# Kernel optimization log

Measured on AMD Instinct MI355X. Metric: run time of the kernel, lower is better.

## Reference

```python
import jax, jax.numpy as jnp
import numpy as np

N = 50000      # nodes
E = 800000     # edges (avg degree 16)
F = 80         # hidden_channels (forced by Linear(80, 1))
L = 4          # num_layers
NG = 1024      # graphs in batch
NFEAT = 9      # OGB atom feature columns
VOCAB = 119    # max atom feature vocab
EPS_BN = 1e-5
EPS_STD = 1e-5


def setup_inputs() -> dict:
    key = jax.random.key(0)
    ks = jax.random.split(key, 20)
    s = 0.05
    x = jax.random.randint(ks[0], (N, NFEAT), 0, 2)
    edge_index = jax.random.randint(ks[1], (2, E), 0, N)
    batch = jnp.sort(jax.random.randint(ks[2], (N,), 0, NG))
    # avg_deg['log'] from the degree histogram == mean over nodes of log(deg+1)
    deg = jax.ops.segment_sum(jnp.ones((E,), jnp.float32), edge_index[1], num_segments=N)
    avg_deg_log = jnp.array([jnp.mean(jnp.log(deg + 1.0))], jnp.float32)
    atom_emb = jax.random.normal(ks[3], (NFEAT, VOCAB, F), jnp.float32) * s
    pre_W = jax.random.normal(ks[4], (L, 2 * F, F), jnp.float32) * s
    pre_b = jax.random.normal(ks[5], (L, F), jnp.float32) * s
    post_W = jax.random.normal(ks[6], (L, 13 * F, F), jnp.float32) * s
    post_b = jax.random.normal(ks[7], (L, F), jnp.float32) * s
    lin_W = jax.random.normal(ks[8], (L, F, F), jnp.float32) * s
    lin_b = jax.random.normal(ks[9], (L, F), jnp.float32) * s
    bn_gamma = 1.0 + jax.random.normal(ks[10], (L, F), jnp.float32) * 0.1
    bn_beta = jax.random.normal(ks[11], (L, F), jnp.float32) * 0.1
    bn_mean = jax.random.normal(ks[12], (L, F), jnp.float32) * 0.1
    bn_var = 0.5 + jax.random.uniform(ks[13], (L, F), jnp.float32)
    mlp_W = jax.random.normal(ks[14], (F, 1), jnp.float32) * s
    mlp_b = jax.random.normal(ks[15], (1,), jnp.float32) * s
    return {
        'x': x, 'edge_index': edge_index, 'batch': batch,
        'avg_deg_log': avg_deg_log, 'atom_emb': atom_emb,
        'pre_W': pre_W, 'pre_b': pre_b, 'post_W': post_W, 'post_b': post_b,
        'lin_W': lin_W, 'lin_b': lin_b,
        'bn_gamma': bn_gamma, 'bn_beta': bn_beta, 'bn_mean': bn_mean, 'bn_var': bn_var,
        'mlp_W': mlp_W, 'mlp_b': mlp_b,
    }


def _forward(x, edge_index, batch, avg_deg_log, atom_emb, pre_W, pre_b,
             post_W, post_b, lin_W, lin_b, bn_gamma, bn_beta, bn_mean, bn_var,
             mlp_W, mlp_b):
    # AtomEncoder: sum of per-column embeddings
    h = jnp.sum(atom_emb[jnp.arange(NFEAT)[None, :], x], axis=1)  # [N, F]
    src, dst = edge_index[0], edge_index[1]
    deg = jax.ops.segment_sum(jnp.ones((E,), h.dtype), dst, num_segments=N)
    has_edge = (deg > 0)[:, None]
    degc = jnp.maximum(deg, 1.0)[:, None]          # clamp(min=1)
    logd = jnp.log(degc + 1.0)                     # [N, 1]
    avg = avg_deg_log[0]
    for i in range(L):
        x_h = h
        # message: pre_nn(cat([x_i, x_j]))
        m = jnp.concatenate([h[dst], h[src]], axis=-1) @ pre_W[i] + pre_b[i]  # [E, F]
        s1 = jax.ops.segment_sum(m, dst, num_segments=N)
        s2 = jax.ops.segment_sum(m * m, dst, num_segments=N)
        mean = s1 / degc
        var = s2 / degc - mean * mean
        std = jnp.sqrt(jax.nn.relu(var) + EPS_STD)
        mn = jnp.where(has_edge, jax.ops.segment_min(m, dst, num_segments=N), 0.0)
        mx = jnp.where(has_edge, jax.ops.segment_max(m, dst, num_segments=N), 0.0)
        agg = jnp.concatenate([mean, mn, mx, std], axis=-1)  # [N, 4F]
        sc = logd / avg
        out = jnp.concatenate([agg, agg * sc, agg / sc], axis=-1)  # [N, 12F]
        out = jnp.concatenate([h, out], axis=-1) @ post_W[i] + post_b[i]  # [N, F]
        out = out @ lin_W[i] + lin_b[i]
        out = (out - bn_mean[i]) * (bn_gamma[i] / jnp.sqrt(bn_var[i] + EPS_BN)) + bn_beta[i]
        h = x_h + jax.nn.relu(out)  # dropout is identity in eval
    counts = jnp.maximum(jax.ops.segment_sum(jnp.ones((N,), h.dtype), batch, num_segments=NG), 1.0)
    g = jax.ops.segment_sum(h, batch, num_segments=NG) / counts[:, None]  # global_mean_pool
    return g @ mlp_W + mlp_b  # [NG, 1]


def reference(x, edge_index, batch, avg_deg_log, atom_emb, pre_W, pre_b,
              post_W, post_b, lin_W, lin_b, bn_gamma, bn_beta, bn_mean, bn_var,
              mlp_W, mlp_b):
    return _forward(x, edge_index, batch, avg_deg_log, atom_emb, pre_W, pre_b,
                    post_W, post_b, lin_W, lin_b, bn_gamma, bn_beta, bn_mean, bn_var,
                    mlp_W, mlp_b)
```

## Files before the change

### kernel.cpp

```cpp
#include <hip/hip_runtime.h>
#include <hip/hip_bf16.h>

#define NN 50000
#define NE 800000
#define FD 80
#define NGR 1024
#define NF 9

#define BSH 6
#define NBUCK ((NN + 63) >> 6)
#define CSH 10
#define NCH ((NE + 1023) >> 10)
#define BCAP 2048

using bf16 = __hip_bfloat16;
typedef __attribute__((ext_vector_type(8))) short bf16x8;
typedef __attribute__((ext_vector_type(4))) float f32x4;

static __device__ __forceinline__ float b2f(bf16 v){ return __bfloat162float(v); }
static __device__ __forceinline__ bf16 f2b(float v){ return __float2bfloat16(v); }
static __device__ __forceinline__ float rdw(const void* p, int i, int fl){
  return fl ? ((const float*)p)[i] : b2f(((const bf16*)p)[i]);
}
static __device__ __forceinline__ unsigned pk(float a, float b){
  bf16 x = f2b(a), y = f2b(b);
  return (unsigned)*(unsigned short*)&x | ((unsigned)*(unsigned short*)&y << 16);
}
static __device__ __forceinline__ bf16x8 ldsld8(const short* p){
  union { bf16x8 v; uint2 u[2]; } r;
  r.u[0] = *(const uint2*)(p);
  r.u[1] = *(const uint2*)(p + 4);
  return r.v;
}
static __device__ __forceinline__ void ldsst16(short* p, uint4 v){
  *(uint2*)(p)     = make_uint2(v.x, v.y);
  *(uint2*)(p + 4) = make_uint2(v.z, v.w);
}

__global__ void k_zero(int* __restrict__ p, int n){
  int t = blockIdx.x*256 + threadIdx.x;
  if (t < n) p[t] = 0;
}

__global__ void k_probe(const void* __restrict__ emb, int* __restrict__ flag){
  int t = blockIdx.x*256 + threadIdx.x;
  float v = b2f(((const bf16*)emb)[t]);
  if (!(fabsf(v) < 1e4f)) atomicOr(flag, 1);
}

__global__ __launch_bounds__(256) void k_prep_all(
    const void* __restrict__ preW, const void* __restrict__ preb,
    const void* __restrict__ postW, const void* __restrict__ postb,
    const void* __restrict__ linW, const void* __restrict__ linb,
    const void* __restrict__ bng, const void* __restrict__ bnb,
    const void* __restrict__ bnm, const void* __restrict__ bnv,
    const int* __restrict__ flag,
    bf16* __restrict__ pwb, bf16* __restrict__ Btl, bf16* __restrict__ Bt1,
    float* __restrict__ bias1, float* __restrict__ bias2)
{
  int fl = flag[0];
  int b = blockIdx.x;
  if (b < 1300){
    int t = b*256 + threadIdx.x;
    pwb[t] = f2b(rdw(postW, t, fl));
  } else if (b < 1420){
    int t = (b - 1300)*256 + threadIdx.x;
    int j = t % 96, c = (t/96) % 80, i = t/(96*80);
    float v = 0.f;
    if (j < 80){
      float gs = rdw(bng, i*80 + c, fl) * rsqrtf(rdw(bnv, i*80 + c, fl) + 1e-5f);
      v = rdw(linW, i*6400 + j*80 + c, fl) * gs;
    }
    Btl[t] = f2b(v);
  } else if (b < 1660){
    int t = (b - 1420)*256 + threadIdx.x;
    int k = t % 96, c = (t/96) % 160, i = t/(96*160);
    float v = 0.f;
    if (k < 80)
      v = (c < 80) ? rdw(preW, (i*160 + k)*80 + c, fl)
                   : rdw(preW, (i*160 + 80 + k)*80 + (c - 80), fl);
    Bt1[t] = f2b(v);
    if (k == 0) bias1[i*160 + c] = (c < 80) ? rdw(preb, i*80 + c, fl) : 0.f;
  } else {
    int t = (b - 1660)*256 + threadIdx.x;
    if (t >= 4*80) return;
    int i = t / 80, f = t - i*80;
    float s = 0.f;
    for (int j = 0; j < 80; j++)
      s += rdw(postb, i*80 + j, fl) * rdw(linW, (i*80 + j)*80 + f, fl);
    s += rdw(linb, t, fl);
    float gs = rdw(bng, t, fl) * rsqrtf(rdw(bnv, t, fl) + 1e-5f);
    bias2[t] = (s - rdw(bnm, t, fl)) * gs + rdw(bnb, t, fl);
  }
}

__global__ void k_prep_Bt2(const float* __restrict__ Wf, bf16* __restrict__ Bt2){
  int t = blockIdx.x*256 + threadIdx.x;
  if (t >= 4*240*416) return;
  int k = t % 416;
  int c = (t/416) % 240;
  int i = t/(416*240);
  float v = 0.f;
  if (k < 400){
    int blk = c/80, f = c - blk*80;
    if (blk == 0) v = Wf[(i*1040 + k)*80 + f];
    else if (k >= 80){
      int row = (blk == 1 ? 400 : 720) + (k - 80);
      v = Wf[(i*1040 + row)*80 + f];
    }
  }
  Bt2[t] = f2b(v);
}

__global__ void k_atom(const int* __restrict__ x, const void* __restrict__ emb,
                       const int* __restrict__ flag, float* __restrict__ h){
  int fl = flag[0];
  int gid = blockIdx.x*256 + threadIdx.x;
  if (gid >= NN*FD) return;
  int n = gid / FD, f = gid - n*FD;
  float s = 0.f;
  #pragma unroll
  for (int c = 0; c < NF; c++){
    int row = x[n*NF + c];
    s += rdw(emb, (c*119 + row)*FD + f, fl);
  }
  h[gid] = s;
}


__global__ __launch_bounds__(256) void k_hist(const int* __restrict__ ei,
                                              int* __restrict__ chunkcnt){
  __shared__ int hist[NBUCK];
  int c = blockIdx.x, t = threadIdx.x;
  for (int i = t; i < NBUCK; i += 256) hist[i] = 0;
  __syncthreads();
  #pragma unroll
  for (int j = 0; j < 4; j++){
    int e = (c << CSH) + j*256 + t;
    if (e < NE) atomicAdd(&hist[ei[NE + e] >> BSH], 1);
  }
  __syncthreads();
  for (int i = t; i < NBUCK; i += 256) chunkcnt[c*NBUCK + i] = hist[i];
}

__global__ __launch_bounds__(256) void k_cscan(int* __restrict__ chunkcnt,
                                               int* __restrict__ btotal){
  __shared__ int buf[256];
  int b = blockIdx.x, t = threadIdx.x;
  int v[4]; int s = 0;
  #pragma unroll
  for (int j = 0; j < 4; j++){
    int c = t*4 + j;
    v[j] = (c < NCH) ? chunkcnt[c*NBUCK + b] : 0;
    s += v[j];
  }
  buf[t] = s;
  __syncthreads();
  for (int off = 1; off < 256; off <<= 1){
    int xv = (t >= off) ? buf[t - off] : 0;
    __syncthreads();
    buf[t] += xv;
    __syncthreads();
  }
  int excl = buf[t] - s;
  #pragma unroll
  for (int j = 0; j < 4; j++){
    int c = t*4 + j;
    if (c < NCH){ chunkcnt[c*NBUCK + b] = excl; excl += v[j]; }
  }
  if (t == 255) btotal[b] = buf[255];
}

__global__ __launch_bounds__(256) void k_bscan(const int* __restrict__ btotal,
                                               int* __restrict__ bbase){
  __shared__ int buf[256];
  int t = threadIdx.x;
  int v[4]; int s = 0;
  #pragma unroll
  for (int j = 0; j < 4; j++){
    int c = t*4 + j;
    v[j] = (c < NBUCK) ? btotal[c] : 0;
    s += v[j];
  }
  buf[t] = s;
  __syncthreads();
  for (int off = 1; off < 256; off <<= 1){
    int xv = (t >= off) ? buf[t - off] : 0;
    __syncthreads();
    buf[t] += xv;
    __syncthreads();
  }
  int excl = buf[t] - s;
  #pragma unroll
  for (int j = 0; j < 4; j++){
    int c = t*4 + j;
    if (c < NBUCK){ bbase[c] = excl; excl += v[j]; }
  }
  if (t == 255) bbase[NBUCK] = buf[255];
}

__global__ __launch_bounds__(256) void k_place(const int* __restrict__ ei,
                        const int* __restrict__ chunkcnt, const int* __restrict__ bbase,
                        int* __restrict__ staging){
  __shared__ int basep[NBUCK];
  __shared__ int cur[NBUCK];
  int c = blockIdx.x, t = threadIdx.x;
  for (int i = t; i < NBUCK; i += 256){
    basep[i] = chunkcnt[c*NBUCK + i] + bbase[i];
    cur[i] = 0;
  }
  __syncthreads();
  #pragma unroll
  for (int j = 0; j < 4; j++){
    int e = (c << CSH) + j*256 + t;
    if (e < NE){
      int d = ei[NE + e], s = ei[e];
      int b = d >> BSH;
      int r = atomicAdd(&cur[b], 1);
      staging[basep[b] + r] = (s << BSH) | (d & 63);
    }
  }
}

__global__ __launch_bounds__(256) void k_csr(const int* __restrict__ staging,
                        const int* __restrict__ bbase, const void* __restrict__ avgp,
                        const int* __restrict__ flag, int* __restrict__ rowptr,
                        float* __restrict__ scf, float* __restrict__ invf,
                        int* __restrict__ colidx){
  __shared__ int lcnt[64], lrp[64], lcur[64];
  __shared__ int colbuf[BCAP];
  int b = blockIdx.x, t = threadIdx.x;
  int base = bbase[b];
  int cnt  = bbase[b+1] - base;
  if (t < 64){ lcnt[t] = 0; lcur[t] = 0; }
  __syncthreads();
  for (int i = t; i < cnt; i += 256)
    atomicAdd(&lcnt[staging[base + i] & 63], 1);
  __syncthreads();
  if (t < 64) lrp[t] = lcnt[t];
  __syncthreads();
  for (int off = 1; off < 64; off <<= 1){
    int xv = (t < 64 && t >= off) ? lrp[t - off] : 0;
    __syncthreads();
    if (t < 64) lrp[t] += xv;
    __syncthreads();
  }
  int n0 = b << BSH;
  if (t < 64){
    int ex = lrp[t] - lcnt[t];
    lrp[t] = ex;
    int n = n0 + t;
    if (n < NN){
      rowptr[n] = base + ex;
      float degc = (float)(lcnt[t] > 0 ? lcnt[t] : 1);
      float logd = logf(degc + 1.f);
      float avg = rdw(avgp, 0, flag[0]);
      scf[n] = logd / avg;
      invf[n] = avg / logd;
    }
  }
  if (b == 0 && t == 0) rowptr[NN] = NE;
  __syncthreads();
  if (cnt <= BCAP){
    for (int i = t; i < cnt; i += 256){
      int v = staging[base + i];
      int l = v & 63;
      int pos = lrp[l] + atomicAdd(&lcur[l], 1);
      colbuf[pos] = v >> BSH;
    }
    __syncthreads();
    for (int i = t; i < cnt; i += 256)
      colidx[base + i] = colbuf[i];
  } else {
    for (int i = t; i < cnt; i += 256){
      int v = staging[base + i];
      int l = v & 63;
      int pos = lrp[l] + atomicAdd(&lcur[l], 1);
      colidx[base + pos] = v >> BSH;
    }
  }
}

template<int AF32, int OUTMODE, int K_, int AST>
__global__ __launch_bounds__(256) void k_mgemm(
    const void* __restrict__ A1p, int s1, int KA,
    const bf16* __restrict__ A2, int s2, int KB,
    const bf16* __restrict__ Btp, int Bts, int Ncols,
    const float* __restrict__ bias,
    void* __restrict__ Cbase, void* __restrict__ Cp2, int Cstride, int M,
    int lA1b, int lBtb, int lCb)
{
  const void* A1 = (const char*)A1p + (size_t)blockIdx.z*lA1b;
  const bf16* Bt = (const bf16*)((const char*)Btp + (size_t)blockIdx.z*lBtb);
  void* Cp = (char*)Cbase + (size_t)blockIdx.z*lCb;

  constexpr int NKT = K_ / 32;
  __shared__ short As[64*AST];
  __shared__ short Bs[256*44];

  const int tid = threadIdx.x;
  const int row0 = blockIdx.x * 64;
  const int wave = tid >> 6, lane = tid & 63;
  const int wc = wave * 64;
  const int m16 = lane & 15, q = lane >> 4;

  const int ra = tid >> 2, ka = (tid & 3) * 8;
  const int cb = tid >> 2, kb = (tid & 3) * 8;

  f32x4 acc[4][4] = {};
  uint4 pb[4];

#define LOADB(k0_) { int kgb = (k0_) + kb;                                     \
    _Pragma("unroll")                                                          \
    for (int j = 0; j < 4; j++){                                               \
      int col = cb + j*64;                                                     \
      pb[j].x = pb[j].y = pb[j].z = pb[j].w = 0u;                              \
      if (col < Ncols) pb[j] = *(const uint4*)(Bt + col*Bts + kgb);            \
    } }

  LOADB(0);

  {
    const int grow = row0 + ra;
    uint4 tA[NKT];
    #pragma unroll
    for (int c = 0; c < NKT; c++){
      int kg = c*32 + ka;
      uint4 pa; pa.x = pa.y = pa.z = pa.w = 0u;
      if (grow < M){
        if (kg < KA){
          if (AF32){
            const float* ap = (const float*)A1 + grow*s1 + kg;
            float4 f0 = *(const float4*)ap;
            float4 f1 = *(const float4*)(ap + 4);
            pa.x = pk(f0.x, f0.y); pa.y = pk(f0.z, f0.w);
            pa.z = pk(f1.x, f1.y); pa.w = pk(f1.z, f1.w);
          } else {
            pa = *(const uint4*)((const bf16*)A1 + grow*s1 + kg);
          }
        } else if (kg - KA < KB){
          pa = *(const uint4*)(A2 + grow*s2 + (kg - KA));
        }
      }
      tA[c] = pa;
    }
    #pragma unroll
    for (int c = 0; c < NKT; c++)
      ldsst16(&As[ra*AST + c*32 + ka], tA[c]);
  }
  __syncthreads();

  #pragma unroll
  for (int ks = 0; ks < NKT; ks++){
    #pragma unroll
    for (int j = 0; j < 4; j++)
      ldsst16(&Bs[(cb + j*64)*44 + kb], pb[j]);
    __syncthreads();

    if (ks + 1 < NKT) LOADB((ks + 1)*32);

    bf16x8 af[4], bfv[4];
    #pragma unroll
    for (int rt = 0; rt < 4; rt++)
      af[rt] = ldsld8(&As[(rt*16 + m16)*AST + ks*32 + q*8]);
    #pragma unroll
    for (int ct = 0; ct < 4; ct++)
      bfv[ct] = ldsld8(&Bs[(wc + ct*16 + m16)*44 + q*8]);
    #pragma unroll
    for (int rt = 0; rt < 4; rt++)
      #pragma unroll
      for (int ct = 0; ct < 4; ct++)
        acc[rt][ct] = __builtin_amdgcn_mfma_f32_16x16x32_bf16(af[rt], bfv[ct], acc[rt][ct], 0, 0, 0);
    __syncthreads();
  }
#undef LOADB

  #pragma unroll
  for (int rt = 0; rt < 4; rt++){
    #pragma unroll
    for (int rr = 0; rr < 4; rr++){
      int row = row0 + rt*16 + q*4 + rr;
      if (row >= M) continue;
      #pragma unroll
      for (int ct = 0; ct < 4; ct++){
        int col = wc + ct*16 + m16;
        if (col >= Ncols) continue;
        float v = acc[rt][ct][rr] + (bias ? bias[col] : 0.f);
        if (OUTMODE == 1) ((float*)Cp)[row*Cstride + col] = v;
        else {
          if (col < 80) ((bf16*)Cp )[row*80 + col]      = f2b(v);
          else          ((bf16*)Cp2)[row*80 + col - 80] = f2b(v);
        }
      }
    }
  }
}

__global__ __launch_bounds__(256) void k_g2(
    const float* __restrict__ h, const bf16* __restrict__ agg,
    const bf16* __restrict__ Bt, const float* __restrict__ bias2v,
    const float* __restrict__ scf, const float* __restrict__ invf,
    float* __restrict__ hp,
    const bf16* __restrict__ Bt1n, const float* __restrict__ bias1n,
    bf16* __restrict__ Ua, bf16* __restrict__ Ub)
{
  constexpr int AST = 420, NKT = 13;
  __shared__ short As[64*AST];
  __shared__ short Bs[256*44];
  bf16* eL = (bf16*)As;
  bf16* hA = (bf16*)(As + 16384);

  const int tid = threadIdx.x;
  const int row0 = blockIdx.x * 64;
  const int wave = tid >> 6, lane = tid & 63;
  const int wc = wave * 64;
  const int m16 = lane & 15, q = lane >> 4;
  const int ra = tid >> 2, ka = (tid & 3) * 8;
  const int cb = tid >> 2, kb = (tid & 3) * 8;

  f32x4 acc[4][4] = {};
  uint4 pb[4];

#define LOADB2(k0_) { int kgb = (k0_) + kb;                                    \
    _Pragma("unroll")                                                          \
    for (int j = 0; j < 4; j++){                                               \
      int col = cb + j*64;                                                     \
      pb[j].x = pb[j].y = pb[j].z = pb[j].w = 0u;                              \
      if (col < 240) pb[j] = *(const uint4*)(Bt + col*416 + kgb);              \
    } }

  LOADB2(0);

  {
    const int grow = row0 + ra;
    uint4 tA[NKT];
    #pragma unroll
    for (int c = 0; c < NKT; c++){
      int kg = c*32 + ka;
      uint4 pa; pa.x = pa.y = pa.z = pa.w = 0u;
      if (grow < NN){
        if (kg < 80){
          const float* ap = h + grow*80 + kg;
          float4 f0 = *(const float4*)ap;
          float4 f1 = *(const float4*)(ap + 4);
          pa.x = pk(f0.x, f0.y); pa.y = pk(f0.z, f0.w);
          pa.z = pk(f1.x, f1.y); pa.w = pk(f1.z, f1.w);
        } else if (kg - 80 < 320){
          pa = *(const uint4*)(agg + grow*320 + (kg - 80));
        }
      }
      tA[c] = pa;
    }
    #pragma unroll
    for (int c = 0; c < NKT; c++)
      ldsst16(&As[ra*AST + c*32 + ka], tA[c]);
  }
  __syncthreads();

  #pragma unroll
  for (int ks = 0; ks < NKT; ks++){
    #pragma unroll
    for (int j = 0; j < 4; j++)
      ldsst16(&Bs[(cb + j*64)*44 + kb], pb[j]);
    __syncthreads();

    if (ks + 1 < NKT) LOADB2((ks + 1)*32);

    bf16x8 af[4], bfv[4];
    #pragma unroll
    for (int rt = 0; rt < 4; rt++)
      af[rt] = ldsld8(&As[(rt*16 + m16)*AST + ks*32 + q*8]);
    #pragma unroll
    for (int ct = 0; ct < 4; ct++)
      bfv[ct] = ldsld8(&Bs[(wc + ct*16 + m16)*44 + q*8]);
    #pragma unroll
    for (int rt = 0; rt < 4; rt++)
      #pragma unroll
      for (int ct = 0; ct < 4; ct++)
        acc[rt][ct] = __builtin_amdgcn_mfma_f32_16x16x32_bf16(af[rt], bfv[ct], acc[rt][ct], 0, 0, 0);
    __syncthreads();
  }
#undef LOADB2

  uint4 pb1[4];
  if (Bt1n){
    #pragma unroll
    for (int j = 0; j < 4; j++){
      int col = cb + j*64;
      pb1[j].x = pb1[j].y = pb1[j].z = pb1[j].w = 0u;
      if (col < 160) pb1[j] = *(const uint4*)(Bt1n + col*96 + kb);
    }
  }

  #pragma unroll
  for (int rt = 0; rt < 4; rt++){
    #pragma unroll
    for (int ct = 0; ct < 4; ct++){
      int col = wc + ct*16 + m16;
      if (col >= 240) continue;
      #pragma unroll
      for (int rr = 0; rr < 4; rr++){
        int r = rt*16 + q*4 + rr;
        eL[r*248 + col] = f2b(acc[rt][ct][rr]);
      }
    }
  }
  __syncthreads();

  #pragma unroll
  for (int i = 0; i < 20; i++){
    int idx = tid + i*256;
    int r = idx / 80, c = idx - r*80;
    int row = row0 + r;
    if (row < NN){
      float P = b2f(eL[r*248 + c]);
      float Q = b2f(eL[r*248 + 80 + c]);
      float R = b2f(eL[r*248 + 160 + c]);
      float o = P + scf[row]*Q + invf[row]*R + bias2v[c];
      float hn = hp[row*80 + c] + fmaxf(o, 0.f);
      hp[row*80 + c] = hn;
      if (Bt1n) hA[r*100 + c] = f2b(hn);
    } else if (Bt1n && idx < 64*80){
      hA[r*100 + c] = f2b(0.f);
    }
  }
  if (Bt1n){
    int r = tid >> 2, off = 80 + (tid & 3)*4;
    *(uint2*)&hA[r*100 + off] = make_uint2(0u, 0u);
  }
  __syncthreads();

  if (Bt1n){
    f32x4 acc2[4][4] = {};
    #pragma unroll
    for (int ks = 0; ks < 3; ks++){
      #pragma unroll
      for (int j = 0; j < 4; j++)
        ldsst16(&Bs[(cb + j*64)*44 + kb], pb1[j]);
      __syncthreads();

      if (ks + 1 < 3){
        int kgb = (ks + 1)*32 + kb;
        #pragma unroll
        for (int j = 0; j < 4; j++){
          int col = cb + j*64;
          pb1[j].x = pb1[j].y = pb1[j].z = pb1[j].w = 0u;
          if (col < 160) pb1[j] = *(const uint4*)(Bt1n + col*96 + kgb);
        }
      }

      bf16x8 af[4], bfv[4];
      #pragma unroll
      for (int rt = 0; rt < 4; rt++)
        af[rt] = ldsld8((const short*)hA + (rt*16 + m16)*100 + ks*32 + q*8);
      #pragma unroll
      for (int ct = 0; ct < 4; ct++)
        bfv[ct] = ldsld8(&Bs[(wc + ct*16 + m16)*44 + q*8]);
      #pragma unroll
      for (int rt = 0; rt < 4; rt++)
        #pragma unroll
        for (int ct = 0; ct < 4; ct++)
          acc2[rt][ct] = __builtin_amdgcn_mfma_f32_16x16x32_bf16(af[rt], bfv[ct], acc2[rt][ct], 0, 0, 0);
      __syncthreads();
    }
    #pragma unroll
    for (int rt = 0; rt < 4; rt++){
      #pragma unroll
      for (int rr = 0; rr < 4; rr++){
        int row = row0 + rt*16 + q*4 + rr;
        if (row >= NN) continue;
        #pragma unroll
        for (int ct = 0; ct < 4; ct++){
          int col = wc + ct*16 + m16;
          if (col >= 160) continue;
          float v = acc2[rt][ct][rr] + bias1n[col];
          if (col < 80) Ua[row*80 + col]      = f2b(v);
          else          Ub[row*80 + col - 80] = f2b(v);
        }
      }
    }
  }
}

__global__ __launch_bounds__(256) void k_agg(const bf16* __restrict__ Ua,
                      const bf16* __restrict__ Ub,
                      const int* __restrict__ rowptr,
                      const int* __restrict__ colidx, bf16* __restrict__ agg)
{
  int lane = threadIdx.x & 63;
  int slot = lane / 20;
  int n = blockIdx.x*12 + (threadIdx.x >> 6)*3 + slot;
  if (slot >= 3 || n >= NN) return;
  int fo = (lane - slot*20) * 4;
  int rs = rowptr[n], re = rowptr[n+1];
  int deg = re - rs;

  float a[4];
  {
    uint2 ua = *(const uint2*)(Ua + n*80 + fo);
    a[0] = __uint_as_float(ua.x << 16);
    a[1] = __uint_as_float(ua.x & 0xffff0000u);
    a[2] = __uint_as_float(ua.y << 16);
    a[3] = __uint_as_float(ua.y & 0xffff0000u);
  }
  float sb[4] = {0.f,0.f,0.f,0.f}, sq[4] = {0.f,0.f,0.f,0.f};
  float mn[4] = {1e30f,1e30f,1e30f,1e30f}, mx[4] = {-1e30f,-1e30f,-1e30f,-1e30f};

#define ACC2(w, o) { \
    float b0 = __uint_as_float((w) << 16); \
    float b1 = __uint_as_float((w) & 0xffff0000u); \
    sb[o] += b0; sq[o] += b0*b0; mn[o] = fminf(mn[o],b0); mx[o] = fmaxf(mx[o],b0); \
    sb[o+1] += b1; sq[o+1] += b1*b1; mn[o+1] = fminf(mn[o+1],b1); mx[o+1] = fmaxf(mx[o+1],b1); }

  for (int e = rs; e < re; e += 8){
    int cnt = re - e; if (cnt > 8) cnt = 8;
    int s[8];
    #pragma unroll
    for (int j = 0; j < 8; j++) s[j] = (j < cnt) ? colidx[e + j] : s[0];
    uint2 u[8];
    #pragma unroll
    for (int j = 0; j < 8; j++) u[j] = *(const uint2*)(Ub + s[j]*80 + fo);
    #pragma unroll
    for (int j = 0; j < 8; j++){
      if (j < cnt){ ACC2(u[j].x, 0); ACC2(u[j].y, 2); }
    }
  }
#undef ACC2

  float degc = (float)(deg > 0 ? deg : 1);
  float inv = 1.f/degc;
  float dm = (float)deg;
  float mean0, mean1, v0, v1, sd0, sd1, lo0, lo1, hi0, hi1;

  mean0 = (dm*a[0] + sb[0])*inv; mean1 = (dm*a[1] + sb[1])*inv;
  v0 = (dm*a[0]*a[0] + 2.f*a[0]*sb[0] + sq[0])*inv - mean0*mean0;
  v1 = (dm*a[1]*a[1] + 2.f*a[1]*sb[1] + sq[1])*inv - mean1*mean1;
  sd0 = sqrtf(fmaxf(v0,0.f)+1e-5f); sd1 = sqrtf(fmaxf(v1,0.f)+1e-5f);
  lo0 = deg>0 ? a[0]+mn[0] : 0.f; lo1 = deg>0 ? a[1]+mn[1] : 0.f;
  hi0 = deg>0 ? a[0]+mx[0] : 0.f; hi1 = deg>0 ? a[1]+mx[1] : 0.f;
  unsigned o0 = pk(mean0, mean1);
  unsigned l0 = pk(lo0, lo1), h0 = pk(hi0, hi1), t0 = pk(sd0, sd1);

  mean0 = (dm*a[2] + sb[2])*inv; mean1 = (dm*a[3] + sb[3])*inv;
  v0 = (dm*a[2]*a[2] + 2.f*a[2]*sb[2] + sq[2])*inv - mean0*mean0;
  v1 = (dm*a[3]*a[3] + 2.f*a[3]*sb[3] + sq[3])*inv - mean1*mean1;
  sd0 = sqrtf(fmaxf(v0,0.f)+1e-5f); sd1 = sqrtf(fmaxf(v1,0.f)+1e-5f);
  lo0 = deg>0 ? a[2]+mn[2] : 0.f; lo1 = deg>0 ? a[3]+mn[3] : 0.f;
  hi0 = deg>0 ? a[2]+mx[2] : 0.f; hi1 = deg>0 ? a[3]+mx[3] : 0.f;
  unsigned o1 = pk(mean0, mean1);
  unsigned l1 = pk(lo0, lo1), h1 = pk(hi0, hi1), t1 = pk(sd0, sd1);

  bf16* ag = agg + n*320 + fo;
  *(uint2*)(ag)       = make_uint2(o0, o1);
  *(uint2*)(ag + 80)  = make_uint2(l0, l1);
  *(uint2*)(ag + 160) = make_uint2(h0, h1);
  *(uint2*)(ag + 240) = make_uint2(t0, t1);
}

__global__ __launch_bounds__(128) void k_poolmlp(const float* __restrict__ h,
                        const int* __restrict__ batch,
                        const void* __restrict__ mlpW, const void* __restrict__ mlpb,
                        const int* __restrict__ flag, void* __restrict__ outp){
  __shared__ float sred[128];
  __shared__ int sb[2];
  int g = blockIdx.x;
  int t = threadIdx.x;
  if (t < 2){
    int target = g + t;
    int lo = 0, hi = NN;
    while (lo < hi){ int mid = (lo + hi) >> 1; if (batch[mid] < target) lo = mid + 1; else hi = mid; }
    sb[t] = lo;
  }
  __syncthreads();
  int lo = sb[0], hi = sb[1];
  float s = 0.f;
  if (t < 80)
    for (int n = lo; n < hi; n++) s += h[n*80 + t];
  int fl = flag[0];
  float wv = (t < 80) ? rdw(mlpW, t, fl) : 0.f;
  sred[t] = s * wv;
  __syncthreads();
  for (int off = 64; off > 0; off >>= 1){
    if (t < off) sred[t] += sred[t + off];
    __syncthreads();
  }
  if (t == 0){
    float cnt = (float)(hi - lo); if (cnt < 1.f) cnt = 1.f;
    float r = sred[0]/cnt + rdw(mlpb, 0, fl);
    if (fl) ((float*)outp)[g] = r;
    else    ((bf16*)outp)[g] = f2b(r);
  }
}

extern "C" void kernel_launch(void* const* d_in, const int* in_sizes, int n_in,
                              void* d_out, int out_size, void* d_ws, size_t ws_size,
                              hipStream_t stream)
{
  const int*  x     = (const int*) d_in[0];
  const int*  ei    = (const int*) d_in[1];
  const int*  batch = (const int*) d_in[2];
  const void* avgp  = d_in[3];
  const void* aemb  = d_in[4];
  const void* preW  = d_in[5];
  const void* preb  = d_in[6];
  const void* postW = d_in[7];
  const void* postb = d_in[8];
  const void* linW  = d_in[9];
  const void* linb  = d_in[10];
  const void* bng   = d_in[11];
  const void* bnb   = d_in[12];
  const void* bnm   = d_in[13];
  const void* bnv   = d_in[14];
  const void* mlpW  = d_in[15];
  const void* mlpb  = d_in[16];

  char* w = (char*)d_ws;
  int*   flag   = (int*)  (w + 400000);
  int*   rowptr = (int*)  (w + 401280);
  int*   colidx = (int*)  (w + 601344);
  float* scf    = (float*)(w + 3801344);
  float* invf   = (float*)(w + 4001344);
  float* bias1  = (float*)(w + 4201344);
  float* bias2  = (float*)(w + 4203904);
  bf16*  Btl    = (bf16*) (w + 4205184);
  bf16*  Bt1    = (bf16*) (w + 4266624);
  bf16*  Bt2    = (bf16*) (w + 4389504);
  float* h      = (float*)(w + 5188224);
  bf16*  Ua     = (bf16*) (w + 21188224);
  bf16*  Ub     = (bf16*) (w + 29188224);
  bf16*  agg    = (bf16*) (w + 45188224);
  bf16*  pwb    = (bf16*) (w + 45188224);
  float* Wf     = (float*)(w + 45853824);
  int* staging  = (int*)  (w + 47185024);
  int* chunkcnt = (int*)  (w + 50385024);
  int* btotal   = (int*)  (w + 52831120);
  int* bbase    = (int*)  (w + 52834248);

  k_zero <<<1, 256, 0, stream>>>(flag, 64);
  k_probe<<<16, 256, 0, stream>>>(aemb, flag);

  k_hist <<<NCH, 256, 0, stream>>>(ei, chunkcnt);
  k_cscan<<<NBUCK, 256, 0, stream>>>(chunkcnt, btotal);
  k_bscan<<<1, 256, 0, stream>>>(btotal, bbase);
  k_place<<<NCH, 256, 0, stream>>>(ei, chunkcnt, bbase, staging);

  k_prep_all<<<1662, 256, 0, stream>>>(preW, preb, postW, postb, linW, linb,
                                       bng, bnb, bnm, bnv, flag,
                                       pwb, Btl, Bt1, bias1, bias2);

  k_mgemm<0,1,96,100><<<dim3(17,1,4), 256, 0, stream>>>(
      pwb, 80, 80, nullptr, 0, 0,
      Btl, 96, 80, nullptr, Wf, nullptr, 80, 1040,
      166400, 15360, 332800);
  k_prep_Bt2<<<(4*240*416 + 255)/256, 256, 0, stream>>>(Wf, Bt2);

  k_atom <<<(NN*FD + 255)/256, 256, 0, stream>>>(x, aemb, flag, h);

  k_csr<<<NBUCK, 256, 0, stream>>>(staging, bbase, avgp, flag, rowptr, scf, invf, colidx);

  const int gx = (NN + 63)/64;
  k_mgemm<1,2,96,100><<<dim3(gx,1,1), 256, 0, stream>>>(
      h, 80, 80, nullptr, 0, 0,
      Bt1, 96, 160, bias1, Ua, Ub, 0, NN,
      0, 0, 0);
  for (int i = 0; i < 4; i++){
    k_agg<<<(NN + 11)/12, 256, 0, stream>>>(Ua, Ub, rowptr, colidx, agg);
    const bf16* nBt1   = (i < 3) ? (Bt1 + (i+1)*15360) : nullptr;
    const float* nb1   = (i < 3) ? (bias1 + (i+1)*160) : bias1;
    k_g2<<<dim3(gx,1,1), 256, 0, stream>>>(
        h, agg, Bt2 + i*99840, bias2 + i*80, scf, invf, h,
        nBt1, nb1, Ua, Ub);
  }

  k_poolmlp<<<NGR, 128, 0, stream>>>(h, batch, mlpW, mlpb, flag, d_out);
}
```

Baseline: 602.1 us.

## Fuse neighbor aggregation into post-GEMM kernel with ping-pong U buffers

The separate aggregation kernel is removed. Each k_g2 block now computes mean/min/max/std over its 64 nodes' neighbors straight into the LDS A tile, staging the block's colidx slice in shared memory when it fits. Ua/Ub become double-buffered, so the next layer's projections do not overwrite neighbor data that other blocks are still reading. This saves the 320-wide agg write and read plus one launch per layer. In exchange, the gather runs with 4 threads per node over 5 serial passes, which means less parallelism and more latency inside the GEMM kernel.

After: 726.4 us. +20.6%, slower.

```diff
diff --git a/kernel.cpp b/kernel.cpp
--- a/kernel.cpp
+++ b/kernel.cpp
@@ -397,16 +397,19 @@
 }
 
 __global__ __launch_bounds__(256) void k_g2(
-    const float* __restrict__ h, const bf16* __restrict__ agg,
+    const float* __restrict__ h,
+    const bf16* __restrict__ Uar, const bf16* __restrict__ Ubr,
+    const int* __restrict__ rowptr, const int* __restrict__ colidx,
     const bf16* __restrict__ Bt, const float* __restrict__ bias2v,
     const float* __restrict__ scf, const float* __restrict__ invf,
     float* __restrict__ hp,
     const bf16* __restrict__ Bt1n, const float* __restrict__ bias1n,
-    bf16* __restrict__ Ua, bf16* __restrict__ Ub)
+    bf16* __restrict__ Uaw, bf16* __restrict__ Ubw)
 {
   constexpr int AST = 420, NKT = 13;
   __shared__ short As[64*AST];
   __shared__ short Bs[256*44];
+  __shared__ int nrp[65];
   bf16* eL = (bf16*)As;
   bf16* hA = (bf16*)(As + 16384);
 
@@ -418,9 +421,107 @@
   const int ra = tid >> 2, ka = (tid & 3) * 8;
   const int cb = tid >> 2, kb = (tid & 3) * 8;
 
-  f32x4 acc[4][4] = {};
+  {
+    int grow = row0 + ra;
+    #pragma unroll
+    for (int c = 0; c < 3; c++){
+      int kg = c*32 + ka;
+      if (kg < 80){
+        uint4 pa; pa.x = pa.y = pa.z = pa.w = 0u;
+        if (grow < NN){
+          const float* ap = h + grow*80 + kg;
+          float4 f0 = *(const float4*)ap;
+          float4 f1 = *(const float4*)(ap + 4);
+          pa.x = pk(f0.x, f0.y); pa.y = pk(f0.z, f0.w);
+          pa.z = pk(f1.x, f1.y); pa.w = pk(f1.z, f1.w);
+        }
+        ldsst16(&As[ra*AST + kg], pa);
+      }
+    }
+    if (ka == 24){
+      uint4 z; z.x = z.y = z.z = z.w = 0u;
+      ldsst16(&As[ra*AST + 400], z);
+      ldsst16(&As[ra*AST + 408], z);
+    }
+  }
+
+  int* ci = (int*)Bs;
+  if (tid < 65){
+    int n = row0 + tid;
+    nrp[tid] = rowptr[n < NN ? n : NN];
+  }
+  __syncthreads();
+  const int e0 = nrp[0];
+  const int ecnt = nrp[64] - e0;
+  const bool inl = (ecnt <= BCAP);
+  if (inl)
+    for (int i = tid; i < ecnt; i += 256) ci[i] = colidx[e0 + i];
+  __syncthreads();
+
+  {
+    int s = tid >> 2, p = tid & 3;
+    int n = row0 + s;
+    int na = n < NN ? n : NN - 1;
+    int rs = nrp[s] - e0, re = nrp[s+1] - e0;
+    int deg = re - rs;
+    float dm = (float)deg;
+    float inv = 1.f / fmaxf(dm, 1.f);
+    short* st = &As[s*AST];
+#define ACCW(w, o) { \
+    float b0 = __uint_as_float((w) << 16); \
+    float b1 = __uint_as_float((w) & 0xffff0000u); \
+    sb[o] += b0; sq[o] += b0*b0; mn[o] = fminf(mn[o],b0); mx[o] = fmaxf(mx[o],b0); \
+    sb[o+1] += b1; sq[o+1] += b1*b1; mn[o+1] = fminf(mn[o+1],b1); mx[o+1] = fmaxf(mx[o+1],b1); }
+    #pragma unroll 1
+    for (int pass = 0; pass < 5; pass++){
+      int fo = pass*16 + p*4;
+      float sb[4] = {0.f,0.f,0.f,0.f}, sq[4] = {0.f,0.f,0.f,0.f};
+      float mn[4] = {1e30f,1e30f,1e30f,1e30f}, mx[4] = {-1e30f,-1e30f,-1e30f,-1e30f};
+      for (int e = rs; e < re; e += 8){
+        int cnb = re - e; if (cnb > 8) cnb = 8;
+        int src[8];
+        #pragma unroll
+        for (int j = 0; j < 8; j++)
+          src[j] = (j < cnb) ? (inl ? ci[e + j] : colidx[e0 + e + j]) : src[0];
+        uint2 u[8];
+        #pragma unroll
+        for (int j = 0; j < 8; j++) u[j] = *(const uint2*)(Ubr + src[j]*80 + fo);
+        #pragma unroll
+        for (int j = 0; j < 8; j++){
+          if (j < cnb){ ACCW(u[j].x, 0); ACCW(u[j].y, 2); }
+        }
+      }
+      float av[4];
+      {
+        uint2 us = *(const uint2*)(Uar + na*80 + fo);
+        av[0] = __uint_as_float(us.x << 16);
+        av[1] = __uint_as_float(us.x & 0xffff0000u);
+        av[2] = __uint_as_float(us.y << 16);
+        av[3] = __uint_as_float(us.y & 0xffff0000u);
+      }
+      float mean[4], lo[4], hi[4], sd[4];
+      #pragma unroll
+      for (int i = 0; i < 4; i++){
+        float a = av[i];
+        mean[i] = (dm*a + sb[i])*inv;
+        float v = (dm*a*a + 2.f*a*sb[i] + sq[i])*inv - mean[i]*mean[i];
+        sd[i] = sqrtf(fmaxf(v, 0.f) + 1e-5f);
+        lo[i] = deg > 0 ? a + mn[i] : 0.f;
+        hi[i] = deg > 0 ? a + mx[i] : 0.f;
+      }
+      *(unsigned*)(st +  80 + fo)     = pk(mean[0], mean[1]);
+      *(unsigned*)(st +  80 + fo + 2) = pk(mean[2], mean[3]);
+      *(unsigned*)(st + 160 + fo)     = pk(lo[0], lo[1]);
+      *(unsigned*)(st + 160 + fo + 2) = pk(lo[2], lo[3]);
+      *(unsigned*)(st + 240 + fo)     = pk(hi[0], hi[1]);
+      *(unsigned*)(st + 240 + fo + 2) = pk(hi[2], hi[3]);
+      *(unsigned*)(st + 320 + fo)     = pk(sd[0], sd[1]);
+      *(unsigned*)(st + 320 + fo + 2) = pk(sd[2], sd[3]);
+    }
+#undef ACCW
+  }
+
   uint4 pb[4];
-
 #define LOADB2(k0_) { int kgb = (k0_) + kb;                                    \
     _Pragma("unroll")                                                          \
     for (int j = 0; j < 4; j++){                                               \
@@ -428,34 +529,10 @@
       pb[j].x = pb[j].y = pb[j].z = pb[j].w = 0u;                              \
       if (col < 240) pb[j] = *(const uint4*)(Bt + col*416 + kgb);              \
     } }
-
   LOADB2(0);
-
-  {
-    const int grow = row0 + ra;
-    uint4 tA[NKT];
-    #pragma unroll
-    for (int c = 0; c < NKT; c++){
-      int kg = c*32 + ka;
-      uint4 pa; pa.x = pa.y = pa.z = pa.w = 0u;
-      if (grow < NN){
-        if (kg < 80){
-          const float* ap = h + grow*80 + kg;
-          float4 f0 = *(const float4*)ap;
-          float4 f1 = *(const float4*)(ap + 4);
-          pa.x = pk(f0.x, f0.y); pa.y = pk(f0.z, f0.w);
-          pa.z = pk(f1.x, f1.y); pa.w = pk(f1.z, f1.w);
-        } else if (kg - 80 < 320){
-          pa = *(const uint4*)(agg + grow*320 + (kg - 80));
-        }
-      }
-      tA[c] = pa;
-    }
-    #pragma unroll
-    for (int c = 0; c < NKT; c++)
-      ldsst16(&As[ra*AST + c*32 + ka], tA[c]);
-  }
-  __syncthreads();
+  __syncthreads();
+
+  f32x4 acc[4][4] = {};
 
   #pragma unroll
   for (int ks = 0; ks < NKT; ks++){
@@ -574,87 +651,12 @@
           int col = wc + ct*16 + m16;
           if (col >= 160) continue;
           float v = acc2[rt][ct][rr] + bias1n[col];
-          if (col < 80) Ua[row*80 + col]      = f2b(v);
-          else          Ub[row*80 + col - 80] = f2b(v);
+          if (col < 80) Uaw[row*80 + col]      = f2b(v);
+          else          Ubw[row*80 + col - 80] = f2b(v);
         }
       }
     }
   }
-}
-
-__global__ __launch_bounds__(256) void k_agg(const bf16* __restrict__ Ua,
-                      const bf16* __restrict__ Ub,
-                      const int* __restrict__ rowptr,
-                      const int* __restrict__ colidx, bf16* __restrict__ agg)
-{
-  int lane = threadIdx.x & 63;
-  int slot = lane / 20;
-  int n = blockIdx.x*12 + (threadIdx.x >> 6)*3 + slot;
-  if (slot >= 3 || n >= NN) return;
-  int fo = (lane - slot*20) * 4;
-  int rs = rowptr[n], re = rowptr[n+1];
-  int deg = re - rs;
-
-  float a[4];
-  {
-    uint2 ua = *(const uint2*)(Ua + n*80 + fo);
-    a[0] = __uint_as_float(ua.x << 16);
-    a[1] = __uint_as_float(ua.x & 0xffff0000u);
-    a[2] = __uint_as_float(ua.y << 16);
-    a[3] = __uint_as_float(ua.y & 0xffff0000u);
-  }
-  float sb[4] = {0.f,0.f,0.f,0.f}, sq[4] = {0.f,0.f,0.f,0.f};
-  float mn[4] = {1e30f,1e30f,1e30f,1e30f}, mx[4] = {-1e30f,-1e30f,-1e30f,-1e30f};
-
-#define ACC2(w, o) { \
-    float b0 = __uint_as_float((w) << 16); \
-    float b1 = __uint_as_float((w) & 0xffff0000u); \
-    sb[o] += b0; sq[o] += b0*b0; mn[o] = fminf(mn[o],b0); mx[o] = fmaxf(mx[o],b0); \
-    sb[o+1] += b1; sq[o+1] += b1*b1; mn[o+1] = fminf(mn[o+1],b1); mx[o+1] = fmaxf(mx[o+1],b1); }
-
-  for (int e = rs; e < re; e += 8){
-    int cnt = re - e; if (cnt > 8) cnt = 8;
-    int s[8];
-    #pragma unroll
-    for (int j = 0; j < 8; j++) s[j] = (j < cnt) ? colidx[e + j] : s[0];
-    uint2 u[8];
-    #pragma unroll
-    for (int j = 0; j < 8; j++) u[j] = *(const uint2*)(Ub + s[j]*80 + fo);
-    #pragma unroll
-    for (int j = 0; j < 8; j++){
-      if (j < cnt){ ACC2(u[j].x, 0); ACC2(u[j].y, 2); }
-    }
-  }
-#undef ACC2
-
-  float degc = (float)(deg > 0 ? deg : 1);
-  float inv = 1.f/degc;
-  float dm = (float)deg;
-  float mean0, mean1, v0, v1, sd0, sd1, lo0, lo1, hi0, hi1;
-
-  mean0 = (dm*a[0] + sb[0])*inv; mean1 = (dm*a[1] + sb[1])*inv;
-  v0 = (dm*a[0]*a[0] + 2.f*a[0]*sb[0] + sq[0])*inv - mean0*mean0;
-  v1 = (dm*a[1]*a[1] + 2.f*a[1]*sb[1] + sq[1])*inv - mean1*mean1;
-  sd0 = sqrtf(fmaxf(v0,0.f)+1e-5f); sd1 = sqrtf(fmaxf(v1,0.f)+1e-5f);
-  lo0 = deg>0 ? a[0]+mn[0] : 0.f; lo1 = deg>0 ? a[1]+mn[1] : 0.f;
-  hi0 = deg>0 ? a[0]+mx[0] : 0.f; hi1 = deg>0 ? a[1]+mx[1] : 0.f;
-  unsigned o0 = pk(mean0, mean1);
-  unsigned l0 = pk(lo0, lo1), h0 = pk(hi0, hi1), t0 = pk(sd0, sd1);
-
-  mean0 = (dm*a[2] + sb[2])*inv; mean1 = (dm*a[3] + sb[3])*inv;
-  v0 = (dm*a[2]*a[2] + 2.f*a[2]*sb[2] + sq[2])*inv - mean0*mean0;
-  v1 = (dm*a[3]*a[3] + 2.f*a[3]*sb[3] + sq[3])*inv - mean1*mean1;
-  sd0 = sqrtf(fmaxf(v0,0.f)+1e-5f); sd1 = sqrtf(fmaxf(v1,0.f)+1e-5f);
-  lo0 = deg>0 ? a[2]+mn[2] : 0.f; lo1 = deg>0 ? a[3]+mn[3] : 0.f;
-  hi0 = deg>0 ? a[2]+mx[2] : 0.f; hi1 = deg>0 ? a[3]+mx[3] : 0.f;
-  unsigned o1 = pk(mean0, mean1);
-  unsigned l1 = pk(lo0, lo1), h1 = pk(hi0, hi1), t1 = pk(sd0, sd1);
-
-  bf16* ag = agg + n*320 + fo;
-  *(uint2*)(ag)       = make_uint2(o0, o1);
-  *(uint2*)(ag + 80)  = make_uint2(l0, l1);
-  *(uint2*)(ag + 160) = make_uint2(h0, h1);
-  *(uint2*)(ag + 240) = make_uint2(t0, t1);
 }
 
 __global__ __launch_bounds__(128) void k_poolmlp(const float* __restrict__ h,
@@ -726,15 +728,16 @@
   bf16*  Bt1    = (bf16*) (w + 4266624);
   bf16*  Bt2    = (bf16*) (w + 4389504);
   float* h      = (float*)(w + 5188224);
-  bf16*  Ua     = (bf16*) (w + 21188224);
-  bf16*  Ub     = (bf16*) (w + 29188224);
-  bf16*  agg    = (bf16*) (w + 45188224);
-  bf16*  pwb    = (bf16*) (w + 45188224);
-  float* Wf     = (float*)(w + 45853824);
-  int* staging  = (int*)  (w + 47185024);
-  int* chunkcnt = (int*)  (w + 50385024);
-  int* btotal   = (int*)  (w + 52831120);
-  int* bbase    = (int*)  (w + 52834248);
+  bf16*  UaA    = (bf16*) (w + 21188224);
+  bf16*  UbA    = (bf16*) (w + 29188224);
+  bf16*  UaB    = (bf16*) (w + 45188224);
+  bf16*  UbB    = (bf16*) (w + 53188224);
+  bf16*  pwb    = (bf16*) (w + 61188224);
+  float* Wf     = (float*)(w + 61853824);
+  int* staging  = (int*)  (w + 63185024);
+  int* chunkcnt = (int*)  (w + 66385024);
+  int* btotal   = (int*)  (w + 68831120);
+  int* bbase    = (int*)  (w + 68834248);
 
   k_zero <<<1, 256, 0, stream>>>(flag, 64);
   k_probe<<<16, 256, 0, stream>>>(aemb, flag);
@@ -761,15 +764,19 @@
   const int gx = (NN + 63)/64;
   k_mgemm<1,2,96,100><<<dim3(gx,1,1), 256, 0, stream>>>(
       h, 80, 80, nullptr, 0, 0,
-      Bt1, 96, 160, bias1, Ua, Ub, 0, NN,
+      Bt1, 96, 160, bias1, UaA, UbA, 0, NN,
       0, 0, 0);
   for (int i = 0; i < 4; i++){
-    k_agg<<<(NN + 11)/12, 256, 0, stream>>>(Ua, Ub, rowptr, colidx, agg);
-    const bf16* nBt1   = (i < 3) ? (Bt1 + (i+1)*15360) : nullptr;
-    const float* nb1   = (i < 3) ? (bias1 + (i+1)*160) : bias1;
+    const bf16* Uar = (i & 1) ? UaB : UaA;
+    const bf16* Ubr = (i & 1) ? UbB : UbA;
+    bf16* Uaw = (i & 1) ? UaA : UaB;
+    bf16* Ubw = (i & 1) ? UbA : UbB;
+    const bf16* nBt1 = (i < 3) ? (Bt1 + (i+1)*15360) : nullptr;
+    const float* nb1 = (i < 3) ? (bias1 + (i+1)*160) : bias1;
     k_g2<<<dim3(gx,1,1), 256, 0, stream>>>(
-        h, agg, Bt2 + i*99840, bias2 + i*80, scf, invf, h,
-        nBt1, nb1, Ua, Ub);
+        h, Uar, Ubr, rowptr, colidx,
+        Bt2 + i*99840, bias2 + i*80, scf, invf, h,
+        nBt1, nb1, Uaw, Ubw);
   }
 
   k_poolmlp<<<NGR, 128, 0, stream>>>(h, batch, mlpW, mlpb, flag, d_out);
```
